# Kernel optimization log

Hardware: AMD Instinct MI355X
Metric: run time of the kernel (lower is better)

Reference implementation:

```python
import jax, jax.numpy as jnp
import numpy as np

DIM = 1024
HEADS = 16
DIM_HEAD = 64
INNER = HEADS * DIM_HEAD
SCALE = DIM_HEAD ** -0.5
CAUSAL = True


def setup_inputs() -> dict:
    key = jax.random.key(0)
    k1, k2, k3, k4 = jax.random.split(key, 4)
    b, n = 4, 2048
    x = jax.random.normal(k1, (b, n, DIM), dtype=jnp.float32)
    mask = jnp.ones((b, n), dtype=bool)
    w_qkv = jax.random.normal(k2, (DIM, 3 * INNER), dtype=jnp.float32) * (DIM ** -0.5)
    w_out = jax.random.normal(k3, (INNER, DIM), dtype=jnp.float32) * (INNER ** -0.5)
    ln_g = jnp.ones((DIM,), dtype=jnp.float32)
    return {"x": x, "mask": mask, "w_qkv": w_qkv, "w_out": w_out, "ln_g": ln_g}


def clip_layernorm(x, g):
    eps = 1e-5 if x.dtype == jnp.float32 else 1e-3
    mean = jnp.mean(x, axis=-1, keepdims=True)
    var = jnp.var(x, axis=-1, keepdims=True)  # unbiased=False
    return (x - mean) * jax.lax.rsqrt(var + eps) * g


def reference(x, mask, w_qkv, w_out, ln_g):
    b, n, _ = x.shape
    qkv = x @ w_qkv  # [b, n, 3*inner]
    q, k, v = jnp.split(qkv, 3, axis=-1)
    split_heads = lambda t: t.reshape(b, n, HEADS, DIM_HEAD).transpose(0, 2, 1, 3)
    q, k, v = split_heads(q), split_heads(k), split_heads(v)
    q = q * SCALE
    sim = jnp.einsum('bhid,bhjd->bhij', q, k)
    mask_value = -jnp.finfo(sim.dtype).max
    sim = jnp.where(mask[:, None, None, :], sim, mask_value)
    if CAUSAL:
        causal_mask = jnp.triu(jnp.ones((n, n), dtype=bool), k=1)
        sim = jnp.where(causal_mask, mask_value, sim)
    attn = jax.nn.softmax(sim.astype(jnp.float32), axis=-1).astype(sim.dtype)
    out = jnp.einsum('bhij,bhjd->bhid', attn, v)
    out = out.transpose(0, 2, 1, 3).reshape(b, n, INNER)
    out = out @ w_out
    return clip_layernorm(out, ln_g)
```

## Files before the change

kernel.cpp:

```cpp
#include <hip/hip_runtime.h>


typedef unsigned short u16;
typedef __attribute__((ext_vector_type(8))) short bf16x8;
typedef __attribute__((ext_vector_type(4))) float f32x4;
typedef __attribute__((ext_vector_type(4))) unsigned short u16x4;
typedef __attribute__((ext_vector_type(2))) unsigned u32x2;

#define B_SZ  4
#define NSEQ  2048
#define DIMM  1024
#define NQKV  3072
#define MROWS 8192

#define AS_GLOBAL __attribute__((address_space(1)))
#define AS_LDS    __attribute__((address_space(3)))

__device__ __forceinline__ void async_copy16(void* lds, const void* g) {
  __builtin_amdgcn_global_load_lds((const AS_GLOBAL void*)g, (AS_LDS void*)lds, 16, 0, 0);
}

__device__ __forceinline__ u16 f32_to_bf16(float f) {
  unsigned u = __float_as_uint(f);
  u += 0x7FFFu + ((u >> 16) & 1u);
  return (u16)(u >> 16);
}

__device__ __forceinline__ unsigned cvt_pk_bf16(float a, float b) {
  unsigned r;
  asm("v_cvt_pk_bf16_f32 %0, %1, %2" : "=v"(r) : "v"(a), "v"(b));
  return r;
}


__global__ __launch_bounds__(256) void cvt_bf16_k(const float* __restrict__ in,
                                                  u16* __restrict__ out, int n4) {
  int i = blockIdx.x * 256 + threadIdx.x;
  if (i >= n4) return;
  f32x4 v = ((const f32x4*)in)[i];
  u16x4 o;
  #pragma unroll
  for (int c = 0; c < 4; ++c) o[c] = f32_to_bf16(v[c]);
  ((u16x4*)out)[i] = o;
}

__global__ __launch_bounds__(256) void tconv_k(const float* __restrict__ in,
                                               u16* __restrict__ out, int K, int N) {
  __shared__ float tile[64][65];
  int n0 = blockIdx.x * 64, k0 = blockIdx.y * 64;
  int t = threadIdx.x, tr = t >> 6, tc = t & 63;
  #pragma unroll
  for (int i = 0; i < 16; ++i)
    tile[tr + i * 4][tc] = in[(size_t)(k0 + tr + i * 4) * N + n0 + tc];
  __syncthreads();
  #pragma unroll
  for (int i = 0; i < 16; ++i)
    out[(size_t)(n0 + tr + i * 4) * K + k0 + tc] = f32_to_bf16(tile[tc][tr + i * 4]);
}


template<int BM, int BN, int NW, int MR>
__device__ __forceinline__ void gemm_loop(const u16* __restrict__ A, const u16* __restrict__ Bt,
                                          int K, size_t arow0, size_t brow0,
                                          u16* lA, u16* lB, f32x4 (&acc)[MR][4]) {
  constexpr int WN  = BN / 64;
  constexpr int MH  = MR / 2;
  constexpr int WTM = 16 * MR;
  constexpr int ASZ = BM * 64;
  constexpr int BSZ = BN * 64;
  const int t = threadIdx.x;
  const int w = t >> 6, lane = t & 63;
  const int l4 = lane >> 4, l15 = lane & 15;
  const int wrow = w / WN, wcol = w % WN;
  const int lr = lane >> 3, lc = lane & 7;

  auto stageA = [&](int kt, int bufi, int h) {
    u16* d = lA + bufi * ASZ;
    #pragma unroll
    for (int j = 0; j < BM / (16 * NW); ++j) {
      int rr = w * (BM / (2 * NW)) + j * 8 + lr;
      int r  = (h + 2 * (rr / (WTM / 2))) * (WTM / 2) + (rr % (WTM / 2));
      async_copy16(&d[(size_t)r * 64 + lc * 8],
                   &A[(arow0 + r) * (size_t)K + kt + (lc ^ (r & 7)) * 8]);
    }
  };
  auto stageB = [&](int kt, int bufi, int h) {
    u16* d = lB + bufi * BSZ;
    #pragma unroll
    for (int j = 0; j < BN / (16 * NW); ++j) {
      int r = h * (BN / 2) + w * (BN / (2 * NW)) + j * 8 + lr;
      async_copy16(&d[(size_t)r * 64 + lc * 8],
                   &Bt[(brow0 + r) * (size_t)K + kt + (lc ^ (r & 7)) * 8]);
    }
  };

  const int T = K >> 6;
  stageA(0, 0, 0); stageB(0, 0, 0); stageB(0, 0, 1); stageA(0, 0, 1);

  #pragma unroll 1
  for (int s = 0; s < T; ++s) {
    const u16* bA = lA + (s & 1) * ASZ;
    const u16* bB = lB + (s & 1) * BSZ;
    const bool st = (s + 1 < T);
    const int kn = (s + 1) * 64, bn = (s + 1) & 1;
    bf16x8 af[MH], bf0[4], bf1[4];

    asm volatile("s_waitcnt vmcnt(2)" ::: "memory");
    __builtin_amdgcn_s_barrier();
    __builtin_amdgcn_sched_barrier(0);
    #pragma unroll
    for (int m = 0; m < MH; ++m) {
      int row = wrow * WTM + m * 16 + l15;
      af[m] = *(const bf16x8*)&bA[(size_t)row * 64 + ((l4) ^ (row & 7)) * 8];
    }
    #pragma unroll
    for (int n = 0; n < 4; ++n) {
      int row = wcol * 64 + n * 16 + l15;
      bf0[n] = *(const bf16x8*)&bB[(size_t)row * 64 + ((l4) ^ (row & 7)) * 8];
      bf1[n] = *(const bf16x8*)&bB[(size_t)row * 64 + ((4 + l4) ^ (row & 7)) * 8];
    }
    if (st) stageA(kn, bn, 0);
    asm volatile("s_waitcnt lgkmcnt(0)" ::: "memory");
    __builtin_amdgcn_sched_barrier(0);
    __builtin_amdgcn_s_setprio(1);
    #pragma unroll
    for (int m = 0; m < MH; ++m)
      #pragma unroll
      for (int n = 0; n < 4; ++n)
        acc[m][n] = __builtin_amdgcn_mfma_f32_16x16x32_bf16(af[m], bf0[n], acc[m][n], 0, 0, 0);
    __builtin_amdgcn_s_setprio(0);
    #pragma unroll
    for (int m = 0; m < MH; ++m) {
      int row = wrow * WTM + m * 16 + l15;
      af[m] = *(const bf16x8*)&bA[(size_t)row * 64 + ((4 + l4) ^ (row & 7)) * 8];
    }
    if (st) stageB(kn, bn, 0);
    asm volatile("s_waitcnt lgkmcnt(0)" ::: "memory");
    __builtin_amdgcn_sched_barrier(0);
    __builtin_amdgcn_s_setprio(1);
    #pragma unroll
    for (int m = 0; m < MH; ++m)
      #pragma unroll
      for (int n = 0; n < 4; ++n)
        acc[m][n] = __builtin_amdgcn_mfma_f32_16x16x32_bf16(af[m], bf1[n], acc[m][n], 0, 0, 0);
    __builtin_amdgcn_s_setprio(0);

    if (st) asm volatile("s_waitcnt vmcnt(4)" ::: "memory");
    else    asm volatile("s_waitcnt vmcnt(0)" ::: "memory");
    __builtin_amdgcn_s_barrier();
    __builtin_amdgcn_sched_barrier(0);
    #pragma unroll
    for (int m = 0; m < MH; ++m) {
      int row = wrow * WTM + (MH + m) * 16 + l15;
      af[m] = *(const bf16x8*)&bA[(size_t)row * 64 + ((l4) ^ (row & 7)) * 8];
    }
    if (st) stageB(kn, bn, 1);
    asm volatile("s_waitcnt lgkmcnt(0)" ::: "memory");
    __builtin_amdgcn_sched_barrier(0);
    __builtin_amdgcn_s_setprio(1);
    #pragma unroll
    for (int m = 0; m < MH; ++m)
      #pragma unroll
      for (int n = 0; n < 4; ++n)
        acc[MH + m][n] = __builtin_amdgcn_mfma_f32_16x16x32_bf16(af[m], bf0[n], acc[MH + m][n], 0, 0, 0);
    __builtin_amdgcn_s_setprio(0);
    #pragma unroll
    for (int m = 0; m < MH; ++m) {
      int row = wrow * WTM + (MH + m) * 16 + l15;
      af[m] = *(const bf16x8*)&bA[(size_t)row * 64 + ((4 + l4) ^ (row & 7)) * 8];
    }
    if (st) stageA(kn, bn, 1);
    asm volatile("s_waitcnt lgkmcnt(0)" ::: "memory");
    __builtin_amdgcn_sched_barrier(0);
    __builtin_amdgcn_s_setprio(1);
    #pragma unroll
    for (int m = 0; m < MH; ++m)
      #pragma unroll
      for (int n = 0; n < 4; ++n)
        acc[MH + m][n] = __builtin_amdgcn_mfma_f32_16x16x32_bf16(af[m], bf1[n], acc[MH + m][n], 0, 0, 0);
    __builtin_amdgcn_s_setprio(0);
  }
}

__global__ __launch_bounds__(512, 2) void gemm_qkv_k(const u16* __restrict__ A, const u16* __restrict__ Bt,
                                                     u16* __restrict__ qb, u16* __restrict__ kb,
                                                     u16* __restrict__ vtb) {
  __shared__ u16 lA[2 * 256 * 64];
  __shared__ u16 lB[2 * 256 * 64];
  f32x4 acc[8][4];
  #pragma unroll
  for (int m = 0; m < 8; ++m)
    #pragma unroll
    for (int n = 0; n < 4; ++n) acc[m][n] = (f32x4){0.f, 0.f, 0.f, 0.f};
  gemm_loop<256, 256, 8, 8>(A, Bt, DIMM, (size_t)blockIdx.y * 256, (size_t)blockIdx.x * 256, lA, lB, acc);
  const int t = threadIdx.x, w = t >> 6, lane = t & 63;
  const int l4 = lane >> 4, l15 = lane & 15;
  const int wrow = w >> 2, wcol = w & 3;
  const float QSCALE = 0.125f * 1.44269504089f;
  #pragma unroll
  for (int m = 0; m < 8; ++m)
    #pragma unroll
    for (int n = 0; n < 4; ++n)
      #pragma unroll
      for (int r = 0; r < 4; ++r) {
        int row = blockIdx.y * 256 + wrow * 128 + m * 16 + l4 * 4 + r;
        int col = blockIdx.x * 256 + wcol * 64 + n * 16 + l15;
        float v = acc[m][n][r];
        int bb = row >> 11, nr = row & 2047;
        int part = col >> 10, rem = col & 1023;
        int h = rem >> 6, d = rem & 63;
        int bh = bb * 16 + h;
        if (part == 0)      qb[((size_t)bh * NSEQ + nr) * 64 + d] = f32_to_bf16(v * QSCALE);
        else if (part == 1) kb[((size_t)bh * NSEQ + nr) * 64 + d] = f32_to_bf16(v);
        else                vtb[((size_t)bh * 64 + d) * NSEQ + nr] = f32_to_bf16(v);
      }
}

__global__ __launch_bounds__(256, 2) void gemm_out_k(const u16* __restrict__ A, const u16* __restrict__ Bt,
                                                     float* __restrict__ C) {
  __shared__ u16 lA[2 * 128 * 64];
  __shared__ u16 lB[2 * 128 * 64];
  f32x4 acc[4][4];
  #pragma unroll
  for (int m = 0; m < 4; ++m)
    #pragma unroll
    for (int n = 0; n < 4; ++n) acc[m][n] = (f32x4){0.f, 0.f, 0.f, 0.f};
  gemm_loop<128, 128, 4, 4>(A, Bt, DIMM, (size_t)blockIdx.y * 128, (size_t)blockIdx.x * 128, lA, lB, acc);
  const int t = threadIdx.x, w = t >> 6, lane = t & 63;
  const int l4 = lane >> 4, l15 = lane & 15;
  const int wrow = w >> 1, wcol = w & 1;
  #pragma unroll
  for (int m = 0; m < 4; ++m)
    #pragma unroll
    for (int n = 0; n < 4; ++n)
      #pragma unroll
      for (int r = 0; r < 4; ++r) {
        int row = blockIdx.y * 128 + wrow * 64 + m * 16 + l4 * 4 + r;
        int col = blockIdx.x * 128 + wcol * 64 + n * 16 + l15;
        C[(size_t)row * DIMM + col] = acc[m][n][r];
      }
}


__global__ __launch_bounds__(512, 4) void attn_k(const u16* __restrict__ qb, const u16* __restrict__ kb,
                                                 const u16* __restrict__ vtb, u16* __restrict__ ao) {
  __shared__ u16 lK[2][64 * 64];
  __shared__ u16 lV[2][64 * 64];
  __shared__ u16 lP[8][16 * 64];
  const int bh = blockIdx.y;
  const int t = threadIdx.x, w = t >> 6, l = t & 63;
  const int l4 = l >> 4, l15 = l & 15;
  const int b = bh >> 4, h = bh & 15;
  u16* lPw = lP[w];

  const int srow = t >> 3;
  const int ssc = (t & 7) ^ (srow & 7);

  #pragma unroll 1
  for (int phase = 0; phase < 2; ++phase) {
    const int qt = phase == 0 ? (int)blockIdx.x : 15 - (int)blockIdx.x;
    const int q0w = qt * 128 + w * 16;

    bf16x8 qf0 = *(const bf16x8*)&qb[((size_t)bh * NSEQ + q0w + l15) * 64 + l4 * 8];
    bf16x8 qf1 = *(const bf16x8*)&qb[((size_t)bh * NSEQ + q0w + l15) * 64 + 32 + l4 * 8];

    float m_r = -1e30f, l_r = 0.f;
    f32x4 o[4];
    #pragma unroll
    for (int d = 0; d < 4; ++d) o[d] = (f32x4){0.f, 0.f, 0.f, 0.f};

    const int njt = 2 * qt + 2;

    {
      async_copy16(&lK[0][t * 8], &kb[((size_t)bh * NSEQ + srow) * 64 + ssc * 8]);
      async_copy16(&lV[0][t * 8], &vtb[((size_t)bh * 64 + srow) * NSEQ + ssc * 8]);
    }
    int buf = 0;

    for (int jt = 0; jt < njt; ++jt) {
      __syncthreads();
      if (jt + 1 < njt) {
        int bsel = buf ^ 1, jn = jt + 1;
        async_copy16(&lK[bsel][t * 8], &kb[((size_t)bh * NSEQ + jn * 64 + srow) * 64 + ssc * 8]);
        async_copy16(&lV[bsel][t * 8], &vtb[((size_t)bh * 64 + srow) * NSEQ + (size_t)jn * 64 + ssc * 8]);
      }
      const int jt64 = jt * 64;
      if (jt64 > q0w + 15) { buf ^= 1; continue; }
      const u16* Kb = lK[buf];
      const u16* Vb = lV[buf];

      bf16x8 kf[4][2];
      #pragma unroll
      for (int nf = 0; nf < 4; ++nf)
        #pragma unroll
        for (int kk = 0; kk < 2; ++kk)
          kf[nf][kk] = *(const bf16x8*)&Kb[(nf * 16 + l15) * 64 + ((kk * 4 + l4) ^ (l15 & 7)) * 8];

      f32x4 z[4];
      __builtin_amdgcn_s_setprio(1);
      #pragma unroll
      for (int nf = 0; nf < 4; ++nf) {
        f32x4 zz = (f32x4){0.f, 0.f, 0.f, 0.f};
        zz = __builtin_amdgcn_mfma_f32_16x16x32_bf16(kf[nf][0], qf0, zz, 0, 0, 0);
        zz = __builtin_amdgcn_mfma_f32_16x16x32_bf16(kf[nf][1], qf1, zz, 0, 0, 0);
        z[nf] = zz;
      }
      __builtin_amdgcn_s_setprio(0);

      bf16x8 bv[4][2];
      #pragma unroll
      for (int dd = 0; dd < 4; ++dd)
        #pragma unroll
        for (int kk = 0; kk < 2; ++kk)
          bv[dd][kk] = *(const bf16x8*)&Vb[(dd * 16 + l15) * 64 + ((kk * 4 + l4) ^ (l15 & 7)) * 8];

      if (jt64 + 63 > q0w) {
        #pragma unroll
        for (int nf = 0; nf < 4; ++nf)
          #pragma unroll
          for (int r = 0; r < 4; ++r)
            if (jt64 + nf * 16 + l4 * 4 + r > q0w + l15) z[nf][r] = -1e30f;
      }

      float mt = fmaxf(fmaxf(z[0][0], z[0][1]), fmaxf(z[0][2], z[0][3]));
      #pragma unroll
      for (int nf = 1; nf < 4; ++nf)
        mt = fmaxf(mt, fmaxf(fmaxf(z[nf][0], z[nf][1]), fmaxf(z[nf][2], z[nf][3])));
      mt = fmaxf(mt, __shfl_xor(mt, 16));
      mt = fmaxf(mt, __shfl_xor(mt, 32));

      if (!__all(mt <= m_r + 8.f)) {
        float nm = fmaxf(m_r, mt);
        float sc = __builtin_amdgcn_exp2f(m_r - nm);
        m_r = nm;
        l_r *= sc;
        float scr[4];
        #pragma unroll
        for (int r = 0; r < 4; ++r) scr[r] = __shfl(sc, l4 * 4 + r);
        #pragma unroll
        for (int d = 0; d < 4; ++d)
          #pragma unroll
          for (int r = 0; r < 4; ++r) o[d][r] *= scr[r];
      }

      float rs = 0.f;
      unsigned pk[4][2];
      #pragma unroll
      for (int nf = 0; nf < 4; ++nf)
        #pragma unroll
        for (int hh = 0; hh < 2; ++hh) {
          float p0 = __builtin_amdgcn_exp2f(z[nf][2 * hh]     - m_r);
          float p1 = __builtin_amdgcn_exp2f(z[nf][2 * hh + 1] - m_r);
          rs += p0 + p1;
          pk[nf][hh] = cvt_pk_bf16(p0, p1);
        }
      rs += __shfl_xor(rs, 16);
      rs += __shfl_xor(rs, 32);
      l_r += rs;

      #pragma unroll
      for (int nf = 0; nf < 4; ++nf) {
        int u = (2 * nf + (l4 >> 1)) ^ (l15 & 7);
        *(u32x2*)&lPw[l15 * 64 + u * 8 + (l4 & 1) * 4] = (u32x2){pk[nf][0], pk[nf][1]};
      }
      __builtin_amdgcn_sched_barrier(0);
      int u0 = l4 ^ (l15 & 7), u1 = (4 + l4) ^ (l15 & 7);
      bf16x8 af0 = *(const bf16x8*)&lPw[l15 * 64 + u0 * 8];
      bf16x8 af1 = *(const bf16x8*)&lPw[l15 * 64 + u1 * 8];

      __builtin_amdgcn_s_setprio(1);
      #pragma unroll
      for (int d = 0; d < 4; ++d) {
        o[d] = __builtin_amdgcn_mfma_f32_16x16x32_bf16(af0, bv[d][0], o[d], 0, 0, 0);
        o[d] = __builtin_amdgcn_mfma_f32_16x16x32_bf16(af1, bv[d][1], o[d], 0, 0, 0);
      }
      __builtin_amdgcn_s_setprio(0);
      buf ^= 1;
    }

    float lv[4];
    #pragma unroll
    for (int r = 0; r < 4; ++r) lv[r] = __shfl(l_r, l4 * 4 + r);
    #pragma unroll
    for (int d = 0; d < 4; ++d)
      #pragma unroll
      for (int r = 0; r < 4; ++r) {
        int nrow = q0w + l4 * 4 + r;
        float vv = o[d][r] / lv[r];
        ao[((size_t)(b * NSEQ + nrow)) * 1024 + h * 64 + d * 16 + l15] = f32_to_bf16(vv);
      }
  }
}

__global__ __launch_bounds__(256) void ln_k(float* __restrict__ io, const float* __restrict__ g) {
  const int row = blockIdx.x, t = threadIdx.x;
  const int w = t >> 6, l = t & 63;
  f32x4 v = ((const f32x4*)(io + (size_t)row * DIMM))[t];
  float s = v[0] + v[1] + v[2] + v[3];
  float q = v[0] * v[0] + v[1] * v[1] + v[2] * v[2] + v[3] * v[3];
  #pragma unroll
  for (int off = 1; off < 64; off <<= 1) { s += __shfl_xor(s, off); q += __shfl_xor(q, off); }
  __shared__ float ss[8];
  if (l == 0) { ss[w] = s; ss[4 + w] = q; }
  __syncthreads();
  s = ss[0] + ss[1] + ss[2] + ss[3];
  q = ss[4] + ss[5] + ss[6] + ss[7];
  float mean = s * (1.f / DIMM);
  float var = q * (1.f / DIMM) - mean * mean;
  float rstd = rsqrtf(var + 1e-5f);
  f32x4 gv = ((const f32x4*)g)[t];
  f32x4 y;
  #pragma unroll
  for (int c = 0; c < 4; ++c) y[c] = (v[c] - mean) * rstd * gv[c];
  ((f32x4*)(io + (size_t)row * DIMM))[t] = y;
}

extern "C" void kernel_launch(void* const* d_in, const int* in_sizes, int n_in,
                              void* d_out, int out_size, void* d_ws, size_t ws_size,
                              hipStream_t stream) {
  const float* x     = (const float*)d_in[0];
  const float* w_qkv = (const float*)d_in[2];
  const float* w_out = (const float*)d_in[3];
  const float* ln_g  = (const float*)d_in[4];
  float* out = (float*)d_out;

  char* ws = (char*)d_ws;
  const size_t MB = 1u << 20;
  u16* x_bf   = (u16*)(ws);
  u16* wqkv_t = (u16*)(ws + 16 * MB);
  u16* wout_t = (u16*)(ws + 22 * MB);
  u16* qb     = (u16*)(ws + 24 * MB);
  u16* kb     = (u16*)(ws + 40 * MB);
  u16* vtb    = (u16*)(ws + 56 * MB);
  u16* attn_o = x_bf;

  cvt_bf16_k<<<8192, 256, 0, stream>>>(x, x_bf, (MROWS * DIMM) / 4);
  tconv_k<<<dim3(NQKV / 64, DIMM / 64), 256, 0, stream>>>(w_qkv, wqkv_t, DIMM, NQKV);
  tconv_k<<<dim3(DIMM / 64, DIMM / 64), 256, 0, stream>>>(w_out, wout_t, DIMM, DIMM);
  gemm_qkv_k<<<dim3(NQKV / 256, MROWS / 256), 512, 0, stream>>>(x_bf, wqkv_t, qb, kb, vtb);
  attn_k<<<dim3(8, B_SZ * 16), 512, 0, stream>>>(qb, kb, vtb, attn_o);
  gemm_out_k<<<dim3(DIMM / 128, MROWS / 128), 256, 0, stream>>>(attn_o, wout_t, out);
  ln_k<<<MROWS, 256, 0, stream>>>(out, ln_g);
}
```

Before: 210.1 us.

## Restructure GEMM main loop with prefetched fragments and swizzle block order

The shared GEMM loop now has one barrier per k-step instead of two. It issues all LDS fragment reads up front and uses partial lgkmcnt waits, so MFMAs can start while later fragment reads are still in flight. The A staging is simplified to contiguous half-tiles, and both GEMM kernels remap block IDs with an XCD-aware swizzle to improve L2 locality. This raises register pressure from the extra fragment arrays and makes the loop wait for all global loads (vmcnt(0)) at the end of each step.

```diff
diff --git a/kernel.cpp b/kernel.cpp
--- a/kernel.cpp
+++ b/kernel.cpp
@@ -30,6 +30,16 @@
   unsigned r;
   asm("v_cvt_pk_bf16_f32 %0, %1, %2" : "=v"(r) : "v"(a), "v"(b));
   return r;
+}
+
+template<int N>
+__device__ __forceinline__ void wait_lgkm() {
+  if constexpr (N == 0)      asm volatile("s_waitcnt lgkmcnt(0)" ::: "memory");
+  else if constexpr (N == 2) asm volatile("s_waitcnt lgkmcnt(2)" ::: "memory");
+  else if constexpr (N == 4) asm volatile("s_waitcnt lgkmcnt(4)" ::: "memory");
+  else if constexpr (N == 6) asm volatile("s_waitcnt lgkmcnt(6)" ::: "memory");
+  else if constexpr (N == 8) asm volatile("s_waitcnt lgkmcnt(8)" ::: "memory");
+  __builtin_amdgcn_sched_barrier(0);
 }
 
 
@@ -78,8 +88,7 @@
     u16* d = lA + bufi * ASZ;
     #pragma unroll
     for (int j = 0; j < BM / (16 * NW); ++j) {
-      int rr = w * (BM / (2 * NW)) + j * 8 + lr;
-      int r  = (h + 2 * (rr / (WTM / 2))) * (WTM / 2) + (rr % (WTM / 2));
+      int r = h * (BM / 2) + w * (BM / (2 * NW)) + j * 8 + lr;
       async_copy16(&d[(size_t)r * 64 + lc * 8],
                    &A[(arow0 + r) * (size_t)K + kt + (lc ^ (r & 7)) * 8]);
     }
@@ -94,8 +103,20 @@
     }
   };
 
+  auto rdA = [&](const u16* bA, int m, int ch) -> bf16x8 {
+    int row = wrow * WTM + m * 16 + l15;
+    return *(const bf16x8*)&bA[(size_t)row * 64 + ((ch + l4) ^ (row & 7)) * 8];
+  };
+  auto rdB = [&](const u16* bB, int n, int ch) -> bf16x8 {
+    int row = wcol * 64 + n * 16 + l15;
+    return *(const bf16x8*)&bB[(size_t)row * 64 + ((ch + l4) ^ (row & 7)) * 8];
+  };
+
   const int T = K >> 6;
   stageA(0, 0, 0); stageB(0, 0, 0); stageB(0, 0, 1); stageA(0, 0, 1);
+  asm volatile("s_waitcnt vmcnt(0)" ::: "memory");
+  __builtin_amdgcn_s_barrier();
+  __builtin_amdgcn_sched_barrier(0);
 
   #pragma unroll 1
   for (int s = 0; s < T; ++s) {
@@ -103,82 +124,65 @@
     const u16* bB = lB + (s & 1) * BSZ;
     const bool st = (s + 1 < T);
     const int kn = (s + 1) * 64, bn = (s + 1) & 1;
-    bf16x8 af[MH], bf0[4], bf1[4];
-
-    asm volatile("s_waitcnt vmcnt(2)" ::: "memory");
+    bf16x8 a0[MH], a1[MH], a2[MH], a3[MH], b0[4], b1[4];
+
+    #pragma unroll
+    for (int m = 0; m < MH; ++m) a0[m] = rdA(bA, m, 0);
+    #pragma unroll
+    for (int n = 0; n < 4; ++n)  b0[n] = rdB(bB, n, 0);
+    #pragma unroll
+    for (int m = 0; m < MH; ++m) a1[m] = rdA(bA, m, 4);
+    #pragma unroll
+    for (int n = 0; n < 4; ++n)  b1[n] = rdB(bB, n, 4);
+    if (st) { stageA(kn, bn, 0); stageB(kn, bn, 0); }
+
+    wait_lgkm<MH + 4>();
+    __builtin_amdgcn_s_setprio(1);
+    #pragma unroll
+    for (int m = 0; m < MH; ++m)
+      #pragma unroll
+      for (int n = 0; n < 4; ++n)
+        acc[m][n] = __builtin_amdgcn_mfma_f32_16x16x32_bf16(a0[m], b0[n], acc[m][n], 0, 0, 0);
+    __builtin_amdgcn_s_setprio(0);
+
+    #pragma unroll
+    for (int m = 0; m < MH; ++m) a2[m] = rdA(bA, MH + m, 0);
+    if (st) stageB(kn, bn, 1);
+
+    wait_lgkm<MH>();
+    __builtin_amdgcn_s_setprio(1);
+    #pragma unroll
+    for (int m = 0; m < MH; ++m)
+      #pragma unroll
+      for (int n = 0; n < 4; ++n)
+        acc[m][n] = __builtin_amdgcn_mfma_f32_16x16x32_bf16(a1[m], b1[n], acc[m][n], 0, 0, 0);
+    __builtin_amdgcn_s_setprio(0);
+
+    #pragma unroll
+    for (int m = 0; m < MH; ++m) a3[m] = rdA(bA, MH + m, 4);
+    if (st) stageA(kn, bn, 1);
+
+    wait_lgkm<MH>();
+    __builtin_amdgcn_s_setprio(1);
+    #pragma unroll
+    for (int m = 0; m < MH; ++m)
+      #pragma unroll
+      for (int n = 0; n < 4; ++n)
+        acc[MH + m][n] = __builtin_amdgcn_mfma_f32_16x16x32_bf16(a2[m], b0[n], acc[MH + m][n], 0, 0, 0);
+    __builtin_amdgcn_s_setprio(0);
+
+    wait_lgkm<0>();
+    __builtin_amdgcn_s_setprio(1);
+    #pragma unroll
+    for (int m = 0; m < MH; ++m)
+      #pragma unroll
+      for (int n = 0; n < 4; ++n)
+        acc[MH + m][n] = __builtin_amdgcn_mfma_f32_16x16x32_bf16(a3[m], b1[n], acc[MH + m][n], 0, 0, 0);
+    __builtin_amdgcn_s_setprio(0);
+
+    asm volatile("s_waitcnt vmcnt(0)" ::: "memory");
     __builtin_amdgcn_s_barrier();
     __builtin_amdgcn_sched_barrier(0);
-    #pragma unroll
-    for (int m = 0; m < MH; ++m) {
-      int row = wrow * WTM + m * 16 + l15;
-      af[m] = *(const bf16x8*)&bA[(size_t)row * 64 + ((l4) ^ (row & 7)) * 8];
-    }
-    #pragma unroll
-    for (int n = 0; n < 4; ++n) {
-      int row = wcol * 64 + n * 16 + l15;
-      bf0[n] = *(const bf16x8*)&bB[(size_t)row * 64 + ((l4) ^ (row & 7)) * 8];
-      bf1[n] = *(const bf16x8*)&bB[(size_t)row * 64 + ((4 + l4) ^ (row & 7)) * 8];
-    }
-    if (st) stageA(kn, bn, 0);
-    asm volatile("s_waitcnt lgkmcnt(0)" ::: "memory");
-    __builtin_amdgcn_sched_barrier(0);
-    __builtin_amdgcn_s_setprio(1);
-    #pragma unroll
-    for (int m = 0; m < MH; ++m)
-      #pragma unroll
-      for (int n = 0; n < 4; ++n)
-        acc[m][n] = __builtin_amdgcn_mfma_f32_16x16x32_bf16(af[m], bf0[n], acc[m][n], 0, 0, 0);
-    __builtin_amdgcn_s_setprio(0);
-    #pragma unroll
-    for (int m = 0; m < MH; ++m) {
-      int row = wrow * WTM + m * 16 + l15;
-      af[m] = *(const bf16x8*)&bA[(size_t)row * 64 + ((4 + l4) ^ (row & 7)) * 8];
-    }
-    if (st) stageB(kn, bn, 0);
-    asm volatile("s_waitcnt lgkmcnt(0)" ::: "memory");
-    __builtin_amdgcn_sched_barrier(0);
-    __builtin_amdgcn_s_setprio(1);
-    #pragma unroll
-    for (int m = 0; m < MH; ++m)
-      #pragma unroll
-      for (int n = 0; n < 4; ++n)
-        acc[m][n] = __builtin_amdgcn_mfma_f32_16x16x32_bf16(af[m], bf1[n], acc[m][n], 0, 0, 0);
-    __builtin_amdgcn_s_setprio(0);
-
-    if (st) asm volatile("s_waitcnt vmcnt(4)" ::: "memory");
-    else    asm volatile("s_waitcnt vmcnt(0)" ::: "memory");
-    __builtin_amdgcn_s_barrier();
-    __builtin_amdgcn_sched_barrier(0);
-    #pragma unroll
-    for (int m = 0; m < MH; ++m) {
-      int row = wrow * WTM + (MH + m) * 16 + l15;
-      af[m] = *(const bf16x8*)&bA[(size_t)row * 64 + ((l4) ^ (row & 7)) * 8];
-    }
-    if (st) stageB(kn, bn, 1);
-    asm volatile("s_waitcnt lgkmcnt(0)" ::: "memory");
-    __builtin_amdgcn_sched_barrier(0);
-    __builtin_amdgcn_s_setprio(1);
-    #pragma unroll
-    for (int m = 0; m < MH; ++m)
-      #pragma unroll
-      for (int n = 0; n < 4; ++n)
-        acc[MH + m][n] = __builtin_amdgcn_mfma_f32_16x16x32_bf16(af[m], bf0[n], acc[MH + m][n], 0, 0, 0);
-    __builtin_amdgcn_s_setprio(0);
-    #pragma unroll
-    for (int m = 0; m < MH; ++m) {
-      int row = wrow * WTM + (MH + m) * 16 + l15;
-      af[m] = *(const bf16x8*)&bA[(size_t)row * 64 + ((4 + l4) ^ (row & 7)) * 8];
-    }
-    if (st) stageA(kn, bn, 1);
-    asm volatile("s_waitcnt lgkmcnt(0)" ::: "memory");
-    __builtin_amdgcn_sched_barrier(0);
-    __builtin_amdgcn_s_setprio(1);
-    #pragma unroll
-    for (int m = 0; m < MH; ++m)
-      #pragma unroll
-      for (int n = 0; n < 4; ++n)
-        acc[MH + m][n] = __builtin_amdgcn_mfma_f32_16x16x32_bf16(af[m], bf1[n], acc[MH + m][n], 0, 0, 0);
-    __builtin_amdgcn_s_setprio(0);
   }
 }
 
@@ -187,12 +191,15 @@
                                                      u16* __restrict__ vtb) {
   __shared__ u16 lA[2 * 256 * 64];
   __shared__ u16 lB[2 * 256 * 64];
+  const int id = (int)blockIdx.y * (NQKV / 256) + (int)blockIdx.x;
+  const int swz = (id & 7) * 48 + (id >> 3);
+  const int bx = swz % (NQKV / 256), by = swz / (NQKV / 256);
   f32x4 acc[8][4];
   #pragma unroll
   for (int m = 0; m < 8; ++m)
     #pragma unroll
     for (int n = 0; n < 4; ++n) acc[m][n] = (f32x4){0.f, 0.f, 0.f, 0.f};
-  gemm_loop<256, 256, 8, 8>(A, Bt, DIMM, (size_t)blockIdx.y * 256, (size_t)blockIdx.x * 256, lA, lB, acc);
+  gemm_loop<256, 256, 8, 8>(A, Bt, DIMM, (size_t)by * 256, (size_t)bx * 256, lA, lB, acc);
   const int t = threadIdx.x, w = t >> 6, lane = t & 63;
   const int l4 = lane >> 4, l15 = lane & 15;
   const int wrow = w >> 2, wcol = w & 3;
@@ -203,8 +210,8 @@
     for (int n = 0; n < 4; ++n)
       #pragma unroll
       for (int r = 0; r < 4; ++r) {
-        int row = blockIdx.y * 256 + wrow * 128 + m * 16 + l4 * 4 + r;
-        int col = blockIdx.x * 256 + wcol * 64 + n * 16 + l15;
+        int row = by * 256 + wrow * 128 + m * 16 + l4 * 4 + r;
+        int col = bx * 256 + wcol * 64 + n * 16 + l15;
         float v = acc[m][n][r];
         int bb = row >> 11, nr = row & 2047;
         int part = col >> 10, rem = col & 1023;
@@ -220,12 +227,15 @@
                                                      float* __restrict__ C) {
   __shared__ u16 lA[2 * 128 * 64];
   __shared__ u16 lB[2 * 128 * 64];
+  const int id = (int)blockIdx.y * (DIMM / 128) + (int)blockIdx.x;
+  const int swz = (id & 7) * 64 + (id >> 3);
+  const int bx = swz % (DIMM / 128), by = swz / (DIMM / 128);
   f32x4 acc[4][4];
   #pragma unroll
   for (int m = 0; m < 4; ++m)
     #pragma unroll
     for (int n = 0; n < 4; ++n) acc[m][n] = (f32x4){0.f, 0.f, 0.f, 0.f};
-  gemm_loop<128, 128, 4, 4>(A, Bt, DIMM, (size_t)blockIdx.y * 128, (size_t)blockIdx.x * 128, lA, lB, acc);
+  gemm_loop<128, 128, 4, 4>(A, Bt, DIMM, (size_t)by * 128, (size_t)bx * 128, lA, lB, acc);
   const int t = threadIdx.x, w = t >> 6, lane = t & 63;
   const int l4 = lane >> 4, l15 = lane & 15;
   const int wrow = w >> 1, wcol = w & 1;
@@ -235,8 +245,8 @@
     for (int n = 0; n < 4; ++n)
       #pragma unroll
       for (int r = 0; r < 4; ++r) {
-        int row = blockIdx.y * 128 + wrow * 64 + m * 16 + l4 * 4 + r;
-        int col = blockIdx.x * 128 + wcol * 64 + n * 16 + l15;
+        int row = by * 128 + wrow * 64 + m * 16 + l4 * 4 + r;
+        int col = bx * 128 + wcol * 64 + n * 16 + l15;
         C[(size_t)row * DIMM + col] = acc[m][n][r];
       }
 }
```

Result: faster. 205.3 us (-2.3%).
